# Performance work log

Hardware: AMD Instinct MI355X
Metric: run time of the kernel (lower is better)

The kernel has to match this reference:

```python
import jax, jax.numpy as jnp
import numpy as np
import math

INPUT_DIM = 2048
OUTPUT_DIM = 8192
SCALE = 1.0


def fwht(x):
    """Fast Walsh-Hadamard transform along the last axis (Sylvester H_n @ x, unnormalized)."""
    n = x.shape[-1]
    orig_shape = x.shape
    x = x.reshape(-1, n)
    h = 1
    while h < n:
        y = x.reshape(x.shape[0], n // (2 * h), 2, h)
        x = jnp.stack([y[:, :, 0] + y[:, :, 1], y[:, :, 0] - y[:, :, 1]], axis=2).reshape(-1, n)
        h *= 2
    return x.reshape(orig_shape)


def setup_inputs() -> dict:
    key = jax.random.key(0)
    kx, kb, kg, ks, kp, ku = jax.random.split(key, 6)
    x = jax.random.normal(kx, (2, 512, 2, INPUT_DIM), dtype=jnp.float32)
    # B: random +/-1 signs (size input_dim)
    B = jnp.where(jax.random.bernoulli(kb, 0.5, (INPUT_DIM,)), 1.0, -1.0).astype(jnp.float32)
    # G: standard normal (size output_dim)
    G = jax.random.normal(kg, (OUTPUT_DIM,), dtype=jnp.float32)
    # S: chi(df=output_dim) samples divided by ||G|| (matches source new_feature_map)
    S = (jnp.sqrt(jax.random.chisquare(ks, OUTPUT_DIM, shape=(OUTPUT_DIM,))).astype(jnp.float32)
         / jnp.linalg.norm(G))
    # P: random permutation of output_dim
    P = jax.random.permutation(kp, OUTPUT_DIM).astype(jnp.int32)
    # U: uniform [0,1); scaled by 2*pi inside reference (phi's random phase)
    U = jax.random.uniform(ku, (OUTPUT_DIM,), dtype=jnp.float32)
    return {"x": x, "B": B, "G": G, "S": S, "P": P, "U": U}


def reference(x, B, G, S, P, U):
    D, O = INPUT_DIM, OUTPUT_DIM
    r = O // D  # repetition, power of 2
    xr = x.reshape(-1, D)                   # (R, D)
    R = xr.shape[0]
    HBx = fwht(xr * B)                      # (R, D): H_D @ (B * x)
    HBx = jnp.tile(HBx, (1, r))             # (R, O): .repeat(1, repetition)
    GPHBx = HBx[:, P] * G                   # (R, O): permute then Gaussian scale
    # stack_hadamard_transforms in the source slices ROWS but transforms the full
    # last dim (length O), so it equals a full-length FWHT on every assigned row.
    HG = fwht(GPHBx)                        # (R, O)
    if R > (r - 1) * D:
        # source leaves the last row unassigned (zeros) in this regime
        HG = HG.at[-1].set(0.0)
    Vx = HG * S * (1.0 / (SCALE * math.sqrt(O)))
    return jnp.cos(Vx + 2.0 * jnp.pi * U) * math.sqrt(2.0 / O)  # (R, O)
```

## Files before the change

### kernel.cpp

```cpp
#include <hip/hip_runtime.h>
#include <math.h>

#define D_IN  2048
#define D_OUT 8192


#if __has_builtin(__builtin_amdgcn_permlane16_swap) && __has_builtin(__builtin_amdgcn_permlane32_swap)
#define HAVE_PLSWAP 1
#endif

template<int CTRL>
__device__ __forceinline__ float dpp_full(float x) {
  int xi = __float_as_int(x);
  return __int_as_float(__builtin_amdgcn_update_dpp(xi, xi, CTRL, 0xF, 0xF, true));
}
__device__ __forceinline__ float dpp_xor4(float x) {
  int xi = __float_as_int(x);
  int r = __builtin_amdgcn_update_dpp(0, xi, 0x124, 0xF, 0xA, false);
  r     = __builtin_amdgcn_update_dpp(r,  xi, 0x12C, 0xF, 0x5, false);
  return __int_as_float(r);
}
__device__ __forceinline__ void bfly_pl16(float& A, float& B, float sgn) {
#ifdef HAVE_PLSWAP
  auto r0 = __builtin_amdgcn_permlane16_swap(__float_as_uint(A), __float_as_uint(B), false, false);
  float lo = __uint_as_float(r0[0]), hi = __uint_as_float(r0[1]);
  float s = lo + hi, d = lo - hi;
  auto r1 = __builtin_amdgcn_permlane16_swap(__float_as_uint(s), __float_as_uint(d), false, false);
  A = __uint_as_float(r1[0]); B = __uint_as_float(r1[1]);
  (void)sgn;
#else
  float pA = __shfl_xor(A, 16, 64); A = fmaf(sgn, A, pA);
  float pB = __shfl_xor(B, 16, 64); B = fmaf(sgn, B, pB);
#endif
}
__device__ __forceinline__ void bfly_pl32(float& A, float& B, float sgn) {
#ifdef HAVE_PLSWAP
  auto r0 = __builtin_amdgcn_permlane32_swap(__float_as_uint(A), __float_as_uint(B), false, false);
  float lo = __uint_as_float(r0[0]), hi = __uint_as_float(r0[1]);
  float s = lo + hi, d = lo - hi;
  auto r1 = __builtin_amdgcn_permlane32_swap(__float_as_uint(s), __float_as_uint(d), false, false);
  A = __uint_as_float(r1[0]); B = __uint_as_float(r1[1]);
  (void)sgn;
#else
  float pA = __shfl_xor(A, 32, 64); A = fmaf(sgn, A, pA);
  float pB = __shfl_xor(B, 32, 64); B = fmaf(sgn, B, pB);
#endif
}

__global__ __launch_bounds__(256) void fastfood_kernel(
    const float* __restrict__ xg, const float* __restrict__ Bg,
    const float* __restrict__ Gg, const float* __restrict__ Sg,
    const int*   __restrict__ Pg, const float* __restrict__ Ug,
    float* __restrict__ outg)
{
  __shared__ float4 X4s[D_OUT / 4];

  const int t = threadIdx.x, lane = t & 63, wave = t >> 6;
  const int row = blockIdx.x;
  const float sg1  = (lane & 1)  ? -1.f : 1.f;
  const float sg2  = (lane & 2)  ? -1.f : 1.f;
  const float sg4  = (lane & 4)  ? -1.f : 1.f;
  const float sg8  = (lane & 8)  ? -1.f : 1.f;
  const float sg16 = (lane & 16) ? -1.f : 1.f;
  const float sg32 = (lane & 32) ? -1.f : 1.f;
  const float s0w = (wave & 1) ? -1.f : 1.f;
  const float s1w = (wave & 2) ? -1.f : 1.f;

  float a[8];
  {
    const float4* x4 = reinterpret_cast<const float4*>(xg + (size_t)row * D_IN);
    const float4* B4 = reinterpret_cast<const float4*>(Bg);
#pragma unroll
    for (int m = 0; m < 2; ++m) {
      int f = lane + 64 * m + 128 * wave;
      float4 xv = x4[f], bv = B4[f];
      a[4*m+0] = xv.x * bv.x; a[4*m+1] = xv.y * bv.y;
      a[4*m+2] = xv.z * bv.z; a[4*m+3] = xv.w * bv.w;
    }
  }
#pragma unroll
  for (int m = 0; m < 2; ++m) {
    float x0=a[4*m],x1=a[4*m+1],x2=a[4*m+2],x3=a[4*m+3];
    float y0=x0+x1,y1=x0-x1,y2=x2+x3,y3=x2-x3;
    a[4*m]=y0+y2; a[4*m+2]=y0-y2; a[4*m+1]=y1+y3; a[4*m+3]=y1-y3;
  }
#pragma unroll
  for (int k = 0; k < 8; ++k) { float p = dpp_full<0xB1>(a[k]);  a[k] = fmaf(sg1, a[k], p); }
#pragma unroll
  for (int k = 0; k < 8; ++k) { float p = dpp_full<0x4E>(a[k]);  a[k] = fmaf(sg2, a[k], p); }
#pragma unroll
  for (int k = 0; k < 8; ++k) { float p = dpp_xor4(a[k]);        a[k] = fmaf(sg4, a[k], p); }
#pragma unroll
  for (int k = 0; k < 8; ++k) { float p = dpp_full<0x128>(a[k]); a[k] = fmaf(sg8, a[k], p); }
#pragma unroll
  for (int k = 0; k < 8; k += 2) bfly_pl16(a[k], a[k+1], sg16);
#pragma unroll
  for (int k = 0; k < 8; k += 2) bfly_pl32(a[k], a[k+1], sg32);
#pragma unroll
  for (int c = 0; c < 4; ++c) {
    float lo = a[c], hi = a[4+c];
    a[c] = lo + hi; a[4+c] = lo - hi;
  }
#pragma unroll
  for (int m = 0; m < 2; ++m)
    X4s[lane + 64 * m + 128 * wave] = make_float4(a[4*m], a[4*m+1], a[4*m+2], a[4*m+3]);
  __syncthreads();
#pragma unroll
  for (int m = 0; m < 2; ++m) {
    int fb = lane + 64 * m;
    float4 B4v = X4s[fb + 128 * (wave ^ 1)];
    float4 C4v = X4s[fb + 128 * (wave ^ 2)];
    float4 D4v = X4s[fb + 128 * (wave ^ 3)];
    float pB[4] = {B4v.x, B4v.y, B4v.z, B4v.w};
    float pC[4] = {C4v.x, C4v.y, C4v.z, C4v.w};
    float pD[4] = {D4v.x, D4v.y, D4v.z, D4v.w};
#pragma unroll
    for (int c = 0; c < 4; ++c) {
      float um = fmaf(s0w, a[4*m+c], pB[c]);
      float uo = fmaf(s0w, pC[c], pD[c]);
      a[4*m+c] = fmaf(s1w, um, uo);
    }
  }
#pragma unroll
  for (int m = 0; m < 2; ++m)
    X4s[1536 + lane + 64 * m + 128 * wave] = make_float4(a[4*m], a[4*m+1], a[4*m+2], a[4*m+3]);
  __syncthreads();

  float v[32];
  {
    const float* a_f = reinterpret_cast<const float*>(X4s + 1536);
    const int4*   P4 = reinterpret_cast<const int4*>(Pg);
    const float4* G4 = reinterpret_cast<const float4*>(Gg);
#pragma unroll
    for (int q = 0; q < 8; ++q) {
      int idx = lane + 64 * q + 512 * wave;
      int4 pp = P4[idx]; float4 gv = G4[idx];
      v[4*q+0] = a_f[pp.x & (D_IN-1)] * gv.x;
      v[4*q+1] = a_f[pp.y & (D_IN-1)] * gv.y;
      v[4*q+2] = a_f[pp.z & (D_IN-1)] * gv.z;
      v[4*q+3] = a_f[pp.w & (D_IN-1)] * gv.w;
    }
  }

#pragma unroll
  for (int q = 0; q < 8; ++q) {
    float x0=v[4*q],x1=v[4*q+1],x2=v[4*q+2],x3=v[4*q+3];
    float y0=x0+x1,y1=x0-x1,y2=x2+x3,y3=x2-x3;
    v[4*q]=y0+y2; v[4*q+2]=y0-y2; v[4*q+1]=y1+y3; v[4*q+3]=y1-y3;
  }
#pragma unroll
  for (int k = 0; k < 32; ++k) { float p = dpp_full<0xB1>(v[k]);  v[k] = fmaf(sg1, v[k], p); }
#pragma unroll
  for (int k = 0; k < 32; ++k) { float p = dpp_full<0x4E>(v[k]);  v[k] = fmaf(sg2, v[k], p); }
#pragma unroll
  for (int k = 0; k < 32; ++k) { float p = dpp_xor4(v[k]);        v[k] = fmaf(sg4, v[k], p); }
#pragma unroll
  for (int k = 0; k < 32; ++k) { float p = dpp_full<0x128>(v[k]); v[k] = fmaf(sg8, v[k], p); }
#pragma unroll
  for (int k = 0; k < 32; k += 2) bfly_pl16(v[k], v[k+1], sg16);
#pragma unroll
  for (int k = 0; k < 32; k += 2) bfly_pl32(v[k], v[k+1], sg32);
#pragma unroll
  for (int b = 1; b < 8; b <<= 1)
#pragma unroll
    for (int q = 0; q < 8; ++q) if (!(q & b))
#pragma unroll
      for (int c = 0; c < 4; ++c) {
        float lo = v[4*q+c], hi = v[4*(q|b)+c];
        v[4*q+c] = lo + hi; v[4*(q|b)+c] = lo - hi;
      }

  __syncthreads();

#pragma unroll
  for (int q = 0; q < 8; ++q)
    X4s[lane + 64 * q + 512 * wave] = make_float4(v[4*q], v[4*q+1], v[4*q+2], v[4*q+3]);
  __syncthreads();
#pragma unroll
  for (int q = 0; q < 8; ++q) {
    int fb = lane + 64 * q;
    float4 B4v = X4s[fb + 512 * (wave ^ 1)];
    float4 C4v = X4s[fb + 512 * (wave ^ 2)];
    float4 D4v = X4s[fb + 512 * (wave ^ 3)];
    float pB[4] = {B4v.x, B4v.y, B4v.z, B4v.w};
    float pC[4] = {C4v.x, C4v.y, C4v.z, C4v.w};
    float pD[4] = {D4v.x, D4v.y, D4v.z, D4v.w};
#pragma unroll
    for (int c = 0; c < 4; ++c) {
      float um = fmaf(s0w, v[4*q+c], pB[c]);
      float uo = fmaf(s0w, pC[c], pD[c]);
      v[4*q+c] = fmaf(s1w, um, uo);
    }
  }

  {
    const float c1 = (float)(1.0 / (6.283185307179586 * 90.50966799187808));
    const float4* S4 = reinterpret_cast<const float4*>(Sg);
    const float4* U4 = reinterpret_cast<const float4*>(Ug);
    float4* out4 = reinterpret_cast<float4*>(outg + (size_t)row * D_OUT);
#pragma unroll
    for (int q = 0; q < 8; ++q) {
      int idx = lane + 64 * q + 512 * wave;
      float4 s4 = S4[idx], u4 = U4[idx], res;
      float rev;
      rev = fmaf(v[4*q+0]*s4.x, c1, u4.x); rev -= rintf(rev); res.x = __builtin_amdgcn_cosf(rev) * 0.015625f;
      rev = fmaf(v[4*q+1]*s4.y, c1, u4.y); rev -= rintf(rev); res.y = __builtin_amdgcn_cosf(rev) * 0.015625f;
      rev = fmaf(v[4*q+2]*s4.z, c1, u4.z); rev -= rintf(rev); res.z = __builtin_amdgcn_cosf(rev) * 0.015625f;
      rev = fmaf(v[4*q+3]*s4.w, c1, u4.w); rev -= rintf(rev); res.w = __builtin_amdgcn_cosf(rev) * 0.015625f;
      out4[idx] = res;
    }
  }
}

extern "C" void kernel_launch(void* const* d_in, const int* in_sizes, int n_in,
                              void* d_out, int out_size, void* d_ws, size_t ws_size,
                              hipStream_t stream) {
  const float* x = (const float*)d_in[0];
  const float* B = (const float*)d_in[1];
  const float* G = (const float*)d_in[2];
  const float* S = (const float*)d_in[3];
  const int*   P = (const int*)d_in[4];
  const float* U = (const float*)d_in[5];
  float* out = (float*)d_out;
  const int rows = in_sizes[0] / D_IN;
  fastfood_kernel<<<rows, 256, 0, stream>>>(x, B, G, S, P, U, out);
}
```

Baseline: 27.64 us.

## Process two rows per block with interleaved stages and compact shared-memory exchange

Each 256-thread block now handles two rows. The second row's small transform and gather are interleaved with the first row's stages so their latencies overlap, and B, P, G, S and U loads are amortised across both rows. Shared memory drops from 32KB to 40KB-per-two-rows through a remapped exchange layout (exqb), and launch bounds request 4 blocks per CU. The risks are higher register pressure from holding two 32-element vectors, which may spill, and half as many blocks in flight. The kernel also assumes an even row count.

```diff
diff --git a/kernel.cpp b/kernel.cpp
--- a/kernel.cpp
+++ b/kernel.cpp
@@ -47,166 +47,214 @@
 #endif
 }
 
-__global__ __launch_bounds__(256) void fastfood_kernel(
+__device__ __forceinline__ void r4grp(float* g) {
+  float y0 = g[0] + g[1], y1 = g[0] - g[1], y2 = g[2] + g[3], y3 = g[2] - g[3];
+  g[0] = y0 + y2; g[2] = y0 - y2; g[1] = y1 + y3; g[3] = y1 - y3;
+}
+template<int N>
+__device__ __forceinline__ void lane_stages(float* v, float sg1, float sg2, float sg4,
+                                            float sg8, float sg16, float sg32) {
+#pragma unroll
+  for (int k = 0; k < N; ++k) { float p = dpp_full<0xB1>(v[k]);  v[k] = fmaf(sg1, v[k], p); }
+#pragma unroll
+  for (int k = 0; k < N; ++k) { float p = dpp_full<0x4E>(v[k]);  v[k] = fmaf(sg2, v[k], p); }
+#pragma unroll
+  for (int k = 0; k < N; ++k) { float p = dpp_xor4(v[k]);        v[k] = fmaf(sg4, v[k], p); }
+#pragma unroll
+  for (int k = 0; k < N; ++k) { float p = dpp_full<0x128>(v[k]); v[k] = fmaf(sg8, v[k], p); }
+#pragma unroll
+  for (int k = 0; k < N; k += 2) bfly_pl16(v[k], v[k+1], sg16);
+#pragma unroll
+  for (int k = 0; k < N; k += 2) bfly_pl32(v[k], v[k+1], sg32);
+}
+template<int NQ>
+__device__ __forceinline__ void reg_stages(float* v) {
+#pragma unroll
+  for (int b = 1; b < NQ; b <<= 1)
+#pragma unroll
+    for (int q = 0; q < NQ; ++q) if (!(q & b))
+#pragma unroll
+      for (int c = 0; c < 4; ++c) {
+        float lo = v[4*q+c], hi = v[4*(q|b)+c];
+        v[4*q+c] = lo + hi; v[4*(q|b)+c] = lo - hi;
+      }
+}
+__device__ __forceinline__ void comb4(float* vq, float4 b4, float4 c4, float4 d4,
+                                      float s0w, float s1w) {
+  float pB[4] = {b4.x, b4.y, b4.z, b4.w};
+  float pC[4] = {c4.x, c4.y, c4.z, c4.w};
+  float pD[4] = {d4.x, d4.y, d4.z, d4.w};
+#pragma unroll
+  for (int c = 0; c < 4; ++c) {
+    float um = fmaf(s0w, vq[c], pB[c]);
+    float uo = fmaf(s0w, pC[c], pD[c]);
+    vq[c] = fmaf(s1w, um, uo);
+  }
+}
+__device__ __forceinline__ int exqb(int w) { return (w == 3) ? 2048 : (w << 9); }
+
+__global__ __launch_bounds__(256, 4) void fastfood_kernel(
     const float* __restrict__ xg, const float* __restrict__ Bg,
     const float* __restrict__ Gg, const float* __restrict__ Sg,
     const int*   __restrict__ Pg, const float* __restrict__ Ug,
     float* __restrict__ outg)
 {
-  __shared__ float4 X4s[D_OUT / 4];
+  __shared__ float4 X4s[2560];
 
   const int t = threadIdx.x, lane = t & 63, wave = t >> 6;
-  const int row = blockIdx.x;
+  const int rowA = 2 * blockIdx.x, rowB = rowA + 1;
   const float sg1  = (lane & 1)  ? -1.f : 1.f;
   const float sg2  = (lane & 2)  ? -1.f : 1.f;
   const float sg4  = (lane & 4)  ? -1.f : 1.f;
   const float sg8  = (lane & 8)  ? -1.f : 1.f;
   const float sg16 = (lane & 16) ? -1.f : 1.f;
   const float sg32 = (lane & 32) ? -1.f : 1.f;
-  const float s0w = (wave & 1) ? -1.f : 1.f;
-  const float s1w = (wave & 2) ? -1.f : 1.f;
-
-  float a[8];
-  {
-    const float4* x4 = reinterpret_cast<const float4*>(xg + (size_t)row * D_IN);
+  const float s0w  = (wave & 1) ? -1.f : 1.f;
+  const float s1w  = (wave & 2) ? -1.f : 1.f;
+  const float c1 = (float)(1.0 / (6.283185307179586 * 90.50966799187808));
+  const int4*   P4 = reinterpret_cast<const int4*>(Pg);
+  const float4* G4 = reinterpret_cast<const float4*>(Gg);
+  const float4* S4 = reinterpret_cast<const float4*>(Sg);
+  const float4* U4 = reinterpret_cast<const float4*>(Ug);
+
+  float a[8], b8[8];
+  {
+    const float4* x4A = reinterpret_cast<const float4*>(xg + (size_t)rowA * D_IN);
+    const float4* x4B = reinterpret_cast<const float4*>(xg + (size_t)rowB * D_IN);
     const float4* B4 = reinterpret_cast<const float4*>(Bg);
 #pragma unroll
     for (int m = 0; m < 2; ++m) {
       int f = lane + 64 * m + 128 * wave;
-      float4 xv = x4[f], bv = B4[f];
-      a[4*m+0] = xv.x * bv.x; a[4*m+1] = xv.y * bv.y;
-      a[4*m+2] = xv.z * bv.z; a[4*m+3] = xv.w * bv.w;
-    }
-  }
-#pragma unroll
-  for (int m = 0; m < 2; ++m) {
-    float x0=a[4*m],x1=a[4*m+1],x2=a[4*m+2],x3=a[4*m+3];
-    float y0=x0+x1,y1=x0-x1,y2=x2+x3,y3=x2-x3;
-    a[4*m]=y0+y2; a[4*m+2]=y0-y2; a[4*m+1]=y1+y3; a[4*m+3]=y1-y3;
-  }
-#pragma unroll
-  for (int k = 0; k < 8; ++k) { float p = dpp_full<0xB1>(a[k]);  a[k] = fmaf(sg1, a[k], p); }
-#pragma unroll
-  for (int k = 0; k < 8; ++k) { float p = dpp_full<0x4E>(a[k]);  a[k] = fmaf(sg2, a[k], p); }
-#pragma unroll
-  for (int k = 0; k < 8; ++k) { float p = dpp_xor4(a[k]);        a[k] = fmaf(sg4, a[k], p); }
-#pragma unroll
-  for (int k = 0; k < 8; ++k) { float p = dpp_full<0x128>(a[k]); a[k] = fmaf(sg8, a[k], p); }
-#pragma unroll
-  for (int k = 0; k < 8; k += 2) bfly_pl16(a[k], a[k+1], sg16);
-#pragma unroll
-  for (int k = 0; k < 8; k += 2) bfly_pl32(a[k], a[k+1], sg32);
-#pragma unroll
-  for (int c = 0; c < 4; ++c) {
-    float lo = a[c], hi = a[4+c];
-    a[c] = lo + hi; a[4+c] = lo - hi;
-  }
+      float4 bv = B4[f], xa = x4A[f], xb = x4B[f];
+      a[4*m+0]  = xa.x * bv.x; a[4*m+1]  = xa.y * bv.y; a[4*m+2]  = xa.z * bv.z; a[4*m+3]  = xa.w * bv.w;
+      b8[4*m+0] = xb.x * bv.x; b8[4*m+1] = xb.y * bv.y; b8[4*m+2] = xb.z * bv.z; b8[4*m+3] = xb.w * bv.w;
+    }
+  }
+  r4grp(a); r4grp(a + 4);
+  lane_stages<8>(a, sg1, sg2, sg4, sg8, sg16, sg32);
+  reg_stages<2>(a);
 #pragma unroll
   for (int m = 0; m < 2; ++m)
     X4s[lane + 64 * m + 128 * wave] = make_float4(a[4*m], a[4*m+1], a[4*m+2], a[4*m+3]);
   __syncthreads();
+
 #pragma unroll
   for (int m = 0; m < 2; ++m) {
     int fb = lane + 64 * m;
-    float4 B4v = X4s[fb + 128 * (wave ^ 1)];
-    float4 C4v = X4s[fb + 128 * (wave ^ 2)];
-    float4 D4v = X4s[fb + 128 * (wave ^ 3)];
-    float pB[4] = {B4v.x, B4v.y, B4v.z, B4v.w};
-    float pC[4] = {C4v.x, C4v.y, C4v.z, C4v.w};
-    float pD[4] = {D4v.x, D4v.y, D4v.z, D4v.w};
-#pragma unroll
-    for (int c = 0; c < 4; ++c) {
-      float um = fmaf(s0w, a[4*m+c], pB[c]);
-      float uo = fmaf(s0w, pC[c], pD[c]);
-      a[4*m+c] = fmaf(s1w, um, uo);
-    }
-  }
-#pragma unroll
-  for (int m = 0; m < 2; ++m)
-    X4s[1536 + lane + 64 * m + 128 * wave] = make_float4(a[4*m], a[4*m+1], a[4*m+2], a[4*m+3]);
-  __syncthreads();
-
-  float v[32];
-  {
-    const float* a_f = reinterpret_cast<const float*>(X4s + 1536);
-    const int4*   P4 = reinterpret_cast<const int4*>(Pg);
-    const float4* G4 = reinterpret_cast<const float4*>(Gg);
+    comb4(a + 4*m, X4s[fb + 128 * (wave ^ 1)], X4s[fb + 128 * (wave ^ 2)],
+          X4s[fb + 128 * (wave ^ 3)], s0w, s1w);
+  }
+#pragma unroll
+  for (int m = 0; m < 2; ++m)
+    X4s[1024 + lane + 64 * m + 128 * wave] = make_float4(a[4*m], a[4*m+1], a[4*m+2], a[4*m+3]);
+  r4grp(b8); r4grp(b8 + 4);
+  lane_stages<8>(b8, sg1, sg2, sg4, sg8, sg16, sg32);
+  reg_stages<2>(b8);
+#pragma unroll
+  for (int m = 0; m < 2; ++m)
+    X4s[512 + lane + 64 * m + 128 * wave] = make_float4(b8[4*m], b8[4*m+1], b8[4*m+2], b8[4*m+3]);
+  __syncthreads();
+
+  float vA[32];
+  {
+    const float* a_f = reinterpret_cast<const float*>(X4s + 1024);
 #pragma unroll
     for (int q = 0; q < 8; ++q) {
       int idx = lane + 64 * q + 512 * wave;
       int4 pp = P4[idx]; float4 gv = G4[idx];
-      v[4*q+0] = a_f[pp.x & (D_IN-1)] * gv.x;
-      v[4*q+1] = a_f[pp.y & (D_IN-1)] * gv.y;
-      v[4*q+2] = a_f[pp.z & (D_IN-1)] * gv.z;
-      v[4*q+3] = a_f[pp.w & (D_IN-1)] * gv.w;
-    }
-  }
-
-#pragma unroll
-  for (int q = 0; q < 8; ++q) {
-    float x0=v[4*q],x1=v[4*q+1],x2=v[4*q+2],x3=v[4*q+3];
-    float y0=x0+x1,y1=x0-x1,y2=x2+x3,y3=x2-x3;
-    v[4*q]=y0+y2; v[4*q+2]=y0-y2; v[4*q+1]=y1+y3; v[4*q+3]=y1-y3;
-  }
-#pragma unroll
-  for (int k = 0; k < 32; ++k) { float p = dpp_full<0xB1>(v[k]);  v[k] = fmaf(sg1, v[k], p); }
-#pragma unroll
-  for (int k = 0; k < 32; ++k) { float p = dpp_full<0x4E>(v[k]);  v[k] = fmaf(sg2, v[k], p); }
-#pragma unroll
-  for (int k = 0; k < 32; ++k) { float p = dpp_xor4(v[k]);        v[k] = fmaf(sg4, v[k], p); }
-#pragma unroll
-  for (int k = 0; k < 32; ++k) { float p = dpp_full<0x128>(v[k]); v[k] = fmaf(sg8, v[k], p); }
-#pragma unroll
-  for (int k = 0; k < 32; k += 2) bfly_pl16(v[k], v[k+1], sg16);
-#pragma unroll
-  for (int k = 0; k < 32; k += 2) bfly_pl32(v[k], v[k+1], sg32);
-#pragma unroll
-  for (int b = 1; b < 8; b <<= 1)
-#pragma unroll
-    for (int q = 0; q < 8; ++q) if (!(q & b))
-#pragma unroll
-      for (int c = 0; c < 4; ++c) {
-        float lo = v[4*q+c], hi = v[4*(q|b)+c];
-        v[4*q+c] = lo + hi; v[4*(q|b)+c] = lo - hi;
-      }
-
-  __syncthreads();
-
-#pragma unroll
-  for (int q = 0; q < 8; ++q)
-    X4s[lane + 64 * q + 512 * wave] = make_float4(v[4*q], v[4*q+1], v[4*q+2], v[4*q+3]);
-  __syncthreads();
-#pragma unroll
-  for (int q = 0; q < 8; ++q) {
-    int fb = lane + 64 * q;
-    float4 B4v = X4s[fb + 512 * (wave ^ 1)];
-    float4 C4v = X4s[fb + 512 * (wave ^ 2)];
-    float4 D4v = X4s[fb + 512 * (wave ^ 3)];
-    float pB[4] = {B4v.x, B4v.y, B4v.z, B4v.w};
-    float pC[4] = {C4v.x, C4v.y, C4v.z, C4v.w};
-    float pD[4] = {D4v.x, D4v.y, D4v.z, D4v.w};
-#pragma unroll
-    for (int c = 0; c < 4; ++c) {
-      float um = fmaf(s0w, v[4*q+c], pB[c]);
-      float uo = fmaf(s0w, pC[c], pD[c]);
-      v[4*q+c] = fmaf(s1w, um, uo);
-    }
-  }
-
-  {
-    const float c1 = (float)(1.0 / (6.283185307179586 * 90.50966799187808));
-    const float4* S4 = reinterpret_cast<const float4*>(Sg);
-    const float4* U4 = reinterpret_cast<const float4*>(Ug);
-    float4* out4 = reinterpret_cast<float4*>(outg + (size_t)row * D_OUT);
+      vA[4*q+0] = a_f[pp.x & (D_IN-1)] * gv.x;
+      vA[4*q+1] = a_f[pp.y & (D_IN-1)] * gv.y;
+      vA[4*q+2] = a_f[pp.z & (D_IN-1)] * gv.z;
+      vA[4*q+3] = a_f[pp.w & (D_IN-1)] * gv.w;
+    }
+  }
+#pragma unroll
+  for (int m = 0; m < 2; ++m) {
+    int fb = lane + 64 * m;
+    comb4(b8 + 4*m, X4s[512 + fb + 128 * (wave ^ 1)], X4s[512 + fb + 128 * (wave ^ 2)],
+          X4s[512 + fb + 128 * (wave ^ 3)], s0w, s1w);
+  }
+#pragma unroll
+  for (int m = 0; m < 2; ++m)
+    X4s[1536 + lane + 64 * m + 128 * wave] = make_float4(b8[4*m], b8[4*m+1], b8[4*m+2], b8[4*m+3]);
+  __syncthreads();
+
+  float vB[32];
+  {
+    const float* b_f = reinterpret_cast<const float*>(X4s + 1536);
+#pragma unroll
+    for (int q = 0; q < 8; ++q) {
+      int idx = lane + 64 * q + 512 * wave;
+      int4 pp = P4[idx]; float4 gv = G4[idx];
+      vB[4*q+0] = b_f[pp.x & (D_IN-1)] * gv.x;
+      vB[4*q+1] = b_f[pp.y & (D_IN-1)] * gv.y;
+      vB[4*q+2] = b_f[pp.z & (D_IN-1)] * gv.z;
+      vB[4*q+3] = b_f[pp.w & (D_IN-1)] * gv.w;
+    }
+  }
+#pragma unroll
+  for (int q = 0; q < 8; ++q) r4grp(vA + 4*q);
+  lane_stages<32>(vA, sg1, sg2, sg4, sg8, sg16, sg32);
+  reg_stages<8>(vA);
+  {
+    int eb = exqb(wave);
+#pragma unroll
+    for (int q = 0; q < 8; ++q)
+      X4s[eb + lane + 64 * q] = make_float4(vA[4*q], vA[4*q+1], vA[4*q+2], vA[4*q+3]);
+  }
+  __syncthreads();
+
+  {
+    int e1 = exqb(wave ^ 1), e2 = exqb(wave ^ 2), e3 = exqb(wave ^ 3);
+#pragma unroll
+    for (int q = 0; q < 8; ++q) {
+      int fb = lane + 64 * q;
+      comb4(vA + 4*q, X4s[e1 + fb], X4s[e2 + fb], X4s[e3 + fb], s0w, s1w);
+    }
+    float4* out4 = reinterpret_cast<float4*>(outg + (size_t)rowA * D_OUT);
 #pragma unroll
     for (int q = 0; q < 8; ++q) {
       int idx = lane + 64 * q + 512 * wave;
       float4 s4 = S4[idx], u4 = U4[idx], res;
       float rev;
-      rev = fmaf(v[4*q+0]*s4.x, c1, u4.x); rev -= rintf(rev); res.x = __builtin_amdgcn_cosf(rev) * 0.015625f;
-      rev = fmaf(v[4*q+1]*s4.y, c1, u4.y); rev -= rintf(rev); res.y = __builtin_amdgcn_cosf(rev) * 0.015625f;
-      rev = fmaf(v[4*q+2]*s4.z, c1, u4.z); rev -= rintf(rev); res.z = __builtin_amdgcn_cosf(rev) * 0.015625f;
-      rev = fmaf(v[4*q+3]*s4.w, c1, u4.w); rev -= rintf(rev); res.w = __builtin_amdgcn_cosf(rev) * 0.015625f;
+      rev = fmaf(vA[4*q+0]*s4.x, c1, u4.x); rev -= rintf(rev); res.x = __builtin_amdgcn_cosf(rev) * 0.015625f;
+      rev = fmaf(vA[4*q+1]*s4.y, c1, u4.y); rev -= rintf(rev); res.y = __builtin_amdgcn_cosf(rev) * 0.015625f;
+      rev = fmaf(vA[4*q+2]*s4.z, c1, u4.z); rev -= rintf(rev); res.z = __builtin_amdgcn_cosf(rev) * 0.015625f;
+      rev = fmaf(vA[4*q+3]*s4.w, c1, u4.w); rev -= rintf(rev); res.w = __builtin_amdgcn_cosf(rev) * 0.015625f;
+      out4[idx] = res;
+    }
+  }
+#pragma unroll
+  for (int q = 0; q < 8; ++q) r4grp(vB + 4*q);
+  lane_stages<32>(vB, sg1, sg2, sg4, sg8, sg16, sg32);
+  reg_stages<8>(vB);
+  __syncthreads();
+
+  {
+    int eb = exqb(wave);
+#pragma unroll
+    for (int q = 0; q < 8; ++q)
+      X4s[eb + lane + 64 * q] = make_float4(vB[4*q], vB[4*q+1], vB[4*q+2], vB[4*q+3]);
+  }
+  __syncthreads();
+
+  {
+    int e1 = exqb(wave ^ 1), e2 = exqb(wave ^ 2), e3 = exqb(wave ^ 3);
+#pragma unroll
+    for (int q = 0; q < 8; ++q) {
+      int fb = lane + 64 * q;
+      comb4(vB + 4*q, X4s[e1 + fb], X4s[e2 + fb], X4s[e3 + fb], s0w, s1w);
+    }
+    float4* out4 = reinterpret_cast<float4*>(outg + (size_t)rowB * D_OUT);
+#pragma unroll
+    for (int q = 0; q < 8; ++q) {
+      int idx = lane + 64 * q + 512 * wave;
+      float4 s4 = S4[idx], u4 = U4[idx], res;
+      float rev;
+      rev = fmaf(vB[4*q+0]*s4.x, c1, u4.x); rev -= rintf(rev); res.x = __builtin_amdgcn_cosf(rev) * 0.015625f;
+      rev = fmaf(vB[4*q+1]*s4.y, c1, u4.y); rev -= rintf(rev); res.y = __builtin_amdgcn_cosf(rev) * 0.015625f;
+      rev = fmaf(vB[4*q+2]*s4.z, c1, u4.z); rev -= rintf(rev); res.z = __builtin_amdgcn_cosf(rev) * 0.015625f;
+      rev = fmaf(vB[4*q+3]*s4.w, c1, u4.w); rev -= rintf(rev); res.w = __builtin_amdgcn_cosf(rev) * 0.015625f;
       out4[idx] = res;
     }
   }
@@ -223,5 +271,5 @@
   const float* U = (const float*)d_in[5];
   float* out = (float*)d_out;
   const int rows = in_sizes[0] / D_IN;
-  fastfood_kernel<<<rows, 256, 0, stream>>>(x, B, G, S, P, U, out);
-}
+  fastfood_kernel<<<rows / 2, 256, 0, stream>>>(x, B, G, S, P, U, out);
+}
```

Result: slower. 59.16 us (+114.0%).
